# Optimization experiments

Measured on AMD Instinct MI355X. Metric: run time of the kernel, lower is better.

The kernel has to match this reference:

```python
import jax, jax.numpy as jnp
import numpy as np

D_MODEL, D_HEAD, N_HEADS, N_KV_HEADS = 4096, 128, 32, 8
EPS = 1e-5
N = 2048


def rms_norm(x, w, eps):
    return x * jax.lax.rsqrt(jnp.mean(x * x, axis=-1, keepdims=True) + eps) * w


def rope_swap(x):
    # [x0, x1, x2, x3] -> [-x1, x0, -x3, x2]
    xp = x.reshape(x.shape[:-1] + (-1, 2))
    return jnp.stack([-xp[..., 1], xp[..., 0]], axis=-1).reshape(x.shape)


def rope_rotate(x, r_cos, r_sin):
    return x * r_cos + rope_swap(x) * r_sin


def setup_inputs() -> dict:
    key = jax.random.key(0)
    ks = jax.random.split(key, 8)
    sd = 1.0 / np.sqrt(D_MODEL)
    return {
        "x": jax.random.normal(ks[0], (N, D_MODEL), dtype=jnp.float32),
        "r_cos": jax.random.normal(ks[1], (N, D_HEAD), dtype=jnp.float32),
        "r_sin": jax.random.normal(ks[2], (N, D_HEAD), dtype=jnp.float32),
        "w_norm": jnp.ones((D_MODEL,), dtype=jnp.float32),
        "wq": jax.random.normal(ks[3], (D_MODEL, N_HEADS * D_HEAD), dtype=jnp.float32) * sd,
        "wk": jax.random.normal(ks[4], (D_MODEL, N_KV_HEADS * D_HEAD), dtype=jnp.float32) * sd,
        "wv": jax.random.normal(ks[5], (D_MODEL, N_KV_HEADS * D_HEAD), dtype=jnp.float32) * sd,
        "wo": jax.random.normal(ks[6], (D_MODEL, D_MODEL), dtype=jnp.float32) * sd,
    }


def reference(x, r_cos, r_sin, w_norm, wq, wk, wv, wo):
    n = x.shape[0]
    residual = x
    h = rms_norm(x, w_norm, EPS)

    # projections -> [n_heads, n, d_head]
    q = (h @ wq).reshape(n, N_HEADS, D_HEAD).transpose(1, 0, 2)
    k = (h @ wk).reshape(n, N_KV_HEADS, D_HEAD).transpose(1, 0, 2)
    v = (h @ wv).reshape(n, N_KV_HEADS, D_HEAD).transpose(1, 0, 2)

    # GQA: repeat kv heads
    reps = N_HEADS // N_KV_HEADS
    k = jnp.repeat(k, reps, axis=0)
    v = jnp.repeat(v, reps, axis=0)

    q = rope_rotate(q, r_cos, r_sin)
    k = rope_rotate(k, r_cos, r_sin)

    mask = jnp.where(
        jnp.tril(jnp.ones((n, n), dtype=bool)), 0.0, -jnp.inf
    ).astype(x.dtype)
    scores = jnp.einsum("hnd,hmd->hnm", q, k) / np.sqrt(D_HEAD).astype(np.float32) + mask
    a = jnp.einsum("hnm,hmd->hnd", jax.nn.softmax(scores, axis=-1), v)

    a = a.transpose(1, 0, 2).reshape(n, N_HEADS * D_HEAD)
    return residual + a @ wo
```

## Files before the change

kernel.cpp:

```cpp
#include <hip/hip_runtime.h>
#include <stdint.h>
#include <math.h>

#define TOK 2048
#define DMODEL 4096
#define QKV_LD 5120
#define KVB 64
#define PS_LD 72

typedef __attribute__((ext_vector_type(8))) short short8;
typedef __attribute__((ext_vector_type(4))) short short4v;
typedef __attribute__((ext_vector_type(8))) __bf16 bf16x8;
typedef __attribute__((ext_vector_type(4))) float f32x4;

__device__ __forceinline__ unsigned short f2bf(float f) {
  unsigned u = __float_as_uint(f);
  u += 0x7fffu + ((u >> 16) & 1u);
  return (unsigned short)(u >> 16);
}

__device__ __forceinline__ void gl16(const void* g, void* l) {
  __builtin_amdgcn_global_load_lds((__attribute__((address_space(1))) void*)g,
                                   (__attribute__((address_space(3))) void*)l,
                                   16, 0, 0);
}

__device__ __forceinline__ f32x4 mfma16(short8 a, short8 b, f32x4 c) {
  return __builtin_amdgcn_mfma_f32_16x16x32_bf16(__builtin_bit_cast(bf16x8, a),
                                                 __builtin_bit_cast(bf16x8, b),
                                                 c, 0, 0, 0);
}

__device__ __forceinline__ float fexp2(float x) {
  float r;
  asm("v_exp_f32 %0, %1" : "=v"(r) : "v"(x));
  return r;
}

template <int N>
__device__ __forceinline__ void waitvm() {
  if constexpr (N == 0) asm volatile("s_waitcnt vmcnt(0)" ::: "memory");
  else if constexpr (N == 6) asm volatile("s_waitcnt vmcnt(6)" ::: "memory");
  else if constexpr (N == 7) asm volatile("s_waitcnt vmcnt(7)" ::: "memory");
  else static_assert(N == 0 || N == 6 || N == 7, "add literal");
}

__global__ __launch_bounds__(256) void k_rmsnorm(const float* __restrict__ x,
                                                 const float* __restrict__ w,
                                                 unsigned short* __restrict__ h) {
  const int row = blockIdx.x;
  const float* xr = x + (size_t)row * DMODEL;
  float4 v[4];
  float ss = 0.f;
#pragma unroll
  for (int i = 0; i < 4; ++i) {
    v[i] = *(const float4*)(xr + threadIdx.x * 4 + i * 1024);
    ss += v[i].x * v[i].x + v[i].y * v[i].y + v[i].z * v[i].z + v[i].w * v[i].w;
  }
#pragma unroll
  for (int m = 1; m < 64; m <<= 1) ss += __shfl_xor(ss, m, 64);
  __shared__ float ws4[4];
  if ((threadIdx.x & 63) == 0) ws4[threadIdx.x >> 6] = ss;
  __syncthreads();
  const float scale = rsqrtf((ws4[0] + ws4[1] + ws4[2] + ws4[3]) * (1.0f / DMODEL) + 1e-5f);
  unsigned short* hr = h + (size_t)row * DMODEL;
#pragma unroll
  for (int i = 0; i < 4; ++i) {
    int col = threadIdx.x * 4 + i * 1024;
    float4 wv = *(const float4*)(w + col);
    uint2 o;
    o.x = (unsigned)f2bf(v[i].x * scale * wv.x) | ((unsigned)f2bf(v[i].y * scale * wv.y) << 16);
    o.y = (unsigned)f2bf(v[i].z * scale * wv.z) | ((unsigned)f2bf(v[i].w * scale * wv.w) << 16);
    *(uint2*)(hr + col) = o;
  }
}

__global__ __launch_bounds__(256) void k_wconvert(const float* __restrict__ W,
                                                  unsigned short* __restrict__ WT,
                                                  int K, int N) {
  __shared__ unsigned short tile[64][65];
  const int n0 = blockIdx.x * 64, k0 = blockIdx.y * 64;
  const int t = threadIdx.x;
  {
    const int r = t >> 2, c0 = (t & 3) * 16;
    const float* src = W + (size_t)(k0 + r) * N + n0 + c0;
#pragma unroll
    for (int i = 0; i < 4; ++i) {
      float4 f = *(const float4*)(src + i * 4);
      tile[r][c0 + i * 4 + 0] = f2bf(f.x);
      tile[r][c0 + i * 4 + 1] = f2bf(f.y);
      tile[r][c0 + i * 4 + 2] = f2bf(f.z);
      tile[r][c0 + i * 4 + 3] = f2bf(f.w);
    }
  }
  __syncthreads();
  {
    const int n = t >> 2, c0 = (t & 3) * 16;
    unsigned short* dst = WT + (size_t)(n0 + n) * K + k0 + c0;
    unsigned short v[16];
#pragma unroll
    for (int i = 0; i < 16; ++i) v[i] = tile[c0 + i][n];
    uint4 o0, o1;
    o0.x = v[0] | ((unsigned)v[1] << 16);  o0.y = v[2] | ((unsigned)v[3] << 16);
    o0.z = v[4] | ((unsigned)v[5] << 16);  o0.w = v[6] | ((unsigned)v[7] << 16);
    o1.x = v[8] | ((unsigned)v[9] << 16);  o1.y = v[10] | ((unsigned)v[11] << 16);
    o1.z = v[12] | ((unsigned)v[13] << 16); o1.w = v[14] | ((unsigned)v[15] << 16);
    *(uint4*)dst = o0;
    *(uint4*)(dst + 8) = o1;
  }
}

__device__ __forceinline__ short8 rdfrag(const unsigned short* buf, int row, int kc) {
  return *(const short8*)((const char*)buf + row * 128 + ((kc ^ (row & 7)) << 4));
}

template <int BM, int BN>
__device__ __forceinline__ void stage_tile(const unsigned short* __restrict__ A,
                                           const unsigned short* __restrict__ BT,
                                           unsigned short* __restrict__ buf,
                                           int m0, int n0, int K, int kt, int tid) {
  constexpr int ALOADS = BM * 8 / 512;
  constexpr int BLOADS = BN * 8 / 512;
  unsigned short* bbuf = buf + BM * 64;
#pragma unroll
  for (int i = 0; i < ALOADS; ++i) {
    const int s = i * 512 + tid, row = s >> 3, ch = s & 7;
    gl16(A + (size_t)(m0 + row) * K + kt + ((ch ^ (row & 7)) << 3), (char*)buf + s * 16);
  }
#pragma unroll
  for (int i = 0; i < BLOADS; ++i) {
    const int s = i * 512 + tid, row = s >> 3, ch = s & 7;
    gl16(BT + (size_t)(n0 + row) * K + kt + ((ch ^ (row & 7)) << 3), (char*)bbuf + s * 16);
  }
}

template <int BM, int BN, int MODE, int GXLOG>
__global__ __launch_bounds__(512, 2) void k_gemm_big(const unsigned short* __restrict__ A,
                                                     const unsigned short* __restrict__ BT,
                                                     const float* __restrict__ resid,
                                                     void* __restrict__ Cout,
                                                     unsigned short* __restrict__ vtg,
                                                     int M, int N, int K) {
  extern __shared__ __align__(16) unsigned short lds[];
  constexpr int MREP = BM / 32;
  constexpr int NREP = BN / 64;
  constexpr int TILE = (BM + BN) * 64;
  constexpr int LOADS = (BM + BN) / 64;

  const int tid = threadIdx.x, lane = tid & 63;
  const int w = tid >> 6, wm = w >> 2, wn = w & 3;
  const int lr = lane & 15, lh = lane >> 4;

  const int nwg = gridDim.x * gridDim.y;
  const int wg0 = blockIdx.y * gridDim.x + blockIdx.x;
  const int swz = (wg0 & 7) * (nwg >> 3) + (wg0 >> 3);
  const int m0 = (swz >> GXLOG) * BM;
  const int n0 = (swz & ((1 << GXLOG) - 1)) * BN;

  const f32x4 zf = {0.f, 0.f, 0.f, 0.f};
  f32x4 acc[MREP][NREP];
#pragma unroll
  for (int i = 0; i < MREP; ++i) {
#pragma unroll
    for (int j = 0; j < NREP; ++j) acc[i][j] = zf;
  }

  const int arow0 = wm * (BM / 2);
  const int brow0 = wn * (BN / 4);
  const int NT = K >> 6;
  int cur = 0;

  stage_tile<BM, BN>(A, BT, lds, m0, n0, K, 0, tid);

  for (int t = 0; t < NT; ++t) {
    const unsigned short* abuf = lds + cur * TILE;
    const unsigned short* bbuf = abuf + BM * 64;
    if (t + 1 < NT) {
      stage_tile<BM, BN>(A, BT, lds + (cur ^ 1) * TILE, m0, n0, K, (t + 1) << 6, tid);
      waitvm<LOADS>();
    } else {
      waitvm<0>();
    }
    __builtin_amdgcn_s_barrier();
    __builtin_amdgcn_sched_barrier(0);

    short8 bfr[NREP][2];
#pragma unroll
    for (int nr = 0; nr < NREP; ++nr) {
#pragma unroll
      for (int kk = 0; kk < 2; ++kk)
        bfr[nr][kk] = rdfrag(bbuf, brow0 + nr * 16 + lr, kk * 4 + lh);
    }
#pragma unroll
    for (int mp = 0; mp < 4; ++mp) {
      short8 afr[2][2];
#pragma unroll
      for (int mi = 0; mi < 2; ++mi) {
#pragma unroll
        for (int kk = 0; kk < 2; ++kk)
          afr[mi][kk] = rdfrag(abuf, arow0 + (mp * 2 + mi) * 16 + lr, kk * 4 + lh);
      }
      __builtin_amdgcn_s_setprio(1);
#pragma unroll
      for (int mi = 0; mi < 2; ++mi) {
#pragma unroll
        for (int nr = 0; nr < NREP; ++nr) {
#pragma unroll
          for (int kk = 0; kk < 2; ++kk)
            acc[mp * 2 + mi][nr] = mfma16(afr[mi][kk], bfr[nr][kk], acc[mp * 2 + mi][nr]);
        }
      }
      __builtin_amdgcn_s_setprio(0);
    }
    __builtin_amdgcn_sched_barrier(0);
    __builtin_amdgcn_s_barrier();
    cur ^= 1;
  }

#pragma unroll
  for (int ai = 0; ai < MREP; ++ai) {
#pragma unroll
    for (int ni = 0; ni < NREP; ++ni) {
      const int colg = n0 + wn * (BN / 4) + ni * 16 + lr;
      const int rowg0 = m0 + wm * (BM / 2) + ai * 16 + 4 * lh;
      if (MODE == 1) {
#pragma unroll
        for (int r = 0; r < 4; ++r)
          ((float*)Cout)[(size_t)(rowg0 + r) * N + colg] =
              acc[ai][ni][r] + resid[(size_t)(rowg0 + r) * N + colg];
      } else if (colg >= 5120) {
        short4v o;
#pragma unroll
        for (int r = 0; r < 4; ++r) o[r] = (short)f2bf(acc[ai][ni][r]);
        *(short4v*)(vtg + (size_t)(colg - 5120) * TOK + rowg0) = o;
      } else {
#pragma unroll
        for (int r = 0; r < 4; ++r)
          ((unsigned short*)Cout)[(size_t)(rowg0 + r) * QKV_LD + colg] = f2bf(acc[ai][ni][r]);
      }
    }
  }
}

__global__ __launch_bounds__(256) void k_rope(unsigned short* __restrict__ qkv,
                                              const float* __restrict__ rc,
                                              const float* __restrict__ rs) {
  const int row = blockIdx.y;
  const int p = blockIdx.x * 256 + threadIdx.x;
  const int col = p * 2;
  const int d = col & 127;
  unsigned short* ptr = qkv + (size_t)row * QKV_LD + col;
  const unsigned both = *(const unsigned*)ptr;
  const float x0 = __uint_as_float((both & 0xffffu) << 16);
  const float x1 = __uint_as_float(both & 0xffff0000u);
  const float c0 = rc[row * 128 + d], c1 = rc[row * 128 + d + 1];
  const float s0 = rs[row * 128 + d], s1 = rs[row * 128 + d + 1];
  const float y0 = x0 * c0 - x1 * s0;
  const float y1 = x1 * c1 + x0 * s1;
  *(unsigned*)ptr = (unsigned)f2bf(y0) | ((unsigned)f2bf(y1) << 16);
}

__global__ __launch_bounds__(256) void k_attn(const unsigned short* __restrict__ qkv,
                                              const unsigned short* __restrict__ vtg,
                                              unsigned short* __restrict__ aout) {
  __shared__ __align__(16) unsigned short Ks[KVB * 128];
  __shared__ __align__(16) unsigned short Vt[128 * KVB];
  __shared__ __align__(16) unsigned short Ps[4][16 * PS_LD];
  const int head = blockIdx.y;
  const int hkv = head >> 2;
  const int tid = threadIdx.x, lane = tid & 63, w = tid >> 6;
  const int lr = lane & 15, lh = lane >> 4;
  const float scale2 = 0.08838834764831845f * 1.44269504088896340736f;
  const f32x4 zf = {0.f, 0.f, 0.f, 0.f};

  for (int half = 0; half < 2; ++half) {
    const int qt = half ? (31 - blockIdx.x) : blockIdx.x;
    const int q0 = qt * 64;

    short8 qf[4];
    {
      const unsigned short* qbase = qkv + (size_t)(q0 + w * 16 + lr) * QKV_LD + head * 128;
#pragma unroll
      for (int kd = 0; kd < 4; ++kd) qf[kd] = *(const short8*)(qbase + kd * 32 + lh * 8);
    }
    f32x4 oacc[8];
#pragma unroll
    for (int vt = 0; vt < 8; ++vt) oacc[vt] = zf;
    float Mr[4], Lr[4];
#pragma unroll
    for (int r = 0; r < 4; ++r) { Mr[r] = -INFINITY; Lr[r] = 0.f; }

    const int nt = qt + 1;
    for (int t = 0; t < nt; ++t) {
      const int kv0 = t * KVB;
      __syncthreads();
#pragma unroll
      for (int c = 0; c < 4; ++c) {
        const int s = c * 256 + w * 64 + lane;
        const int row = s >> 4, cp = s & 15;
        gl16(qkv + (size_t)(kv0 + row) * QKV_LD + 4096 + hkv * 128 + ((cp ^ (row & 7)) * 8),
             (char*)Ks + (c * 256 + w * 64) * 16);
      }
#pragma unroll
      for (int c = 0; c < 4; ++c) {
        const int s = c * 256 + w * 64 + lane;
        const int row = s >> 3, cp = s & 7;
        gl16(vtg + (size_t)(hkv * 128 + row) * TOK + kv0 + ((cp ^ (row & 7)) * 8),
             (char*)Vt + (c * 256 + w * 64) * 16);
      }
      __syncthreads();

      f32x4 sacc[4];
#pragma unroll
      for (int ct = 0; ct < 4; ++ct) {
        sacc[ct] = zf;
        const int row = ct * 16 + lr;
#pragma unroll
        for (int kd = 0; kd < 4; ++kd) {
          const short8 kf = *(const short8*)((const char*)Ks + row * 256 +
                                             (((kd * 4 + lh) ^ (row & 7)) * 16));
          sacc[ct] = mfma16(qf[kd], kf, sacc[ct]);
        }
      }

      float scv[4], pv[4][4];
#pragma unroll
      for (int r = 0; r < 4; ++r) {
        const int qrow = q0 + w * 16 + 4 * lh + r;
        float s0 = sacc[0][r] * scale2;
        float s1 = sacc[1][r] * scale2;
        float s2 = sacc[2][r] * scale2;
        float s3 = sacc[3][r] * scale2;
        if (kv0 + lr > qrow) s0 = -INFINITY;
        if (kv0 + 16 + lr > qrow) s1 = -INFINITY;
        if (kv0 + 32 + lr > qrow) s2 = -INFINITY;
        if (kv0 + 48 + lr > qrow) s3 = -INFINITY;
        float tmax = fmaxf(fmaxf(s0, s1), fmaxf(s2, s3));
        tmax = fmaxf(tmax, __shfl_xor(tmax, 1, 16));
        tmax = fmaxf(tmax, __shfl_xor(tmax, 2, 16));
        tmax = fmaxf(tmax, __shfl_xor(tmax, 4, 16));
        tmax = fmaxf(tmax, __shfl_xor(tmax, 8, 16));
        const float mnew = fmaxf(Mr[r], tmax);
        const float sc = fexp2(Mr[r] - mnew);
        Mr[r] = mnew;
        const float p0 = fexp2(s0 - mnew);
        const float p1 = fexp2(s1 - mnew);
        const float p2 = fexp2(s2 - mnew);
        const float p3 = fexp2(s3 - mnew);
        float ps = (p0 + p1) + (p2 + p3);
        ps += __shfl_xor(ps, 1, 16);
        ps += __shfl_xor(ps, 2, 16);
        ps += __shfl_xor(ps, 4, 16);
        ps += __shfl_xor(ps, 8, 16);
        Lr[r] = Lr[r] * sc + ps;
        scv[r] = sc;
        pv[r][0] = p0; pv[r][1] = p1; pv[r][2] = p2; pv[r][3] = p3;
      }
#pragma unroll
      for (int vt = 0; vt < 8; ++vt) {
#pragma unroll
        for (int r = 0; r < 4; ++r) oacc[vt][r] *= scv[r];
      }

      unsigned short* pw = Ps[w];
#pragma unroll
      for (int r = 0; r < 4; ++r) {
#pragma unroll
        for (int ct = 0; ct < 4; ++ct)
          pw[(4 * lh + r) * PS_LD + ct * 16 + lr] = f2bf(pv[r][ct]);
      }
      asm volatile("s_waitcnt lgkmcnt(0)" ::: "memory");
      short8 pf[2];
      pf[0] = *(const short8*)(pw + lr * PS_LD + lh * 8);
      pf[1] = *(const short8*)(pw + lr * PS_LD + 32 + lh * 8);
      __builtin_amdgcn_s_setprio(1);
#pragma unroll
      for (int vt = 0; vt < 8; ++vt) {
        const int d = vt * 16 + lr;
#pragma unroll
        for (int kb = 0; kb < 2; ++kb) {
          const short8 vf = *(const short8*)((const char*)Vt + d * 128 +
                                             (((kb * 4 + lh) ^ (lr & 7)) * 16));
          oacc[vt] = mfma16(pf[kb], vf, oacc[vt]);
        }
      }
      __builtin_amdgcn_s_setprio(0);
    }

#pragma unroll
    for (int r = 0; r < 4; ++r) {
      const float inv = 1.0f / Lr[r];
      const size_t rowoff = (size_t)(q0 + w * 16 + 4 * lh + r) * DMODEL + head * 128;
#pragma unroll
      for (int vt = 0; vt < 8; ++vt)
        aout[rowoff + vt * 16 + lr] = f2bf(oacc[vt][r] * inv);
    }
  }
}

extern "C" void kernel_launch(void* const* d_in, const int* in_sizes, int n_in,
                              void* d_out, int out_size, void* d_ws, size_t ws_size,
                              hipStream_t stream) {
  (void)in_sizes; (void)n_in; (void)out_size; (void)ws_size;
  const float* x     = (const float*)d_in[0];
  const float* r_cos = (const float*)d_in[1];
  const float* r_sin = (const float*)d_in[2];
  const float* wnorm = (const float*)d_in[3];
  const float* wq    = (const float*)d_in[4];
  const float* wk    = (const float*)d_in[5];
  const float* wv    = (const float*)d_in[6];
  const float* wo    = (const float*)d_in[7];

  unsigned short* bufA = (unsigned short*)d_ws;
  unsigned short* qkvb = bufA + (size_t)TOK * DMODEL;
  unsigned short* wT   = qkvb + (size_t)TOK * QKV_LD;
  unsigned short* vtg  = wT + (size_t)6144 * DMODEL;

  hipFuncSetAttribute((const void*)k_gemm_big<256, 192, 0, 5>,
                      hipFuncAttributeMaxDynamicSharedMemorySize, 4 * (256 + 192) * 64);
  hipFuncSetAttribute((const void*)k_gemm_big<256, 128, 1, 5>,
                      hipFuncAttributeMaxDynamicSharedMemorySize, 4 * (256 + 128) * 64);

  k_rmsnorm<<<TOK, 256, 0, stream>>>(x, wnorm, bufA);
  k_wconvert<<<dim3(64, 64), 256, 0, stream>>>(wq, wT, DMODEL, 4096);
  k_wconvert<<<dim3(16, 64), 256, 0, stream>>>(wk, wT + (size_t)4096 * DMODEL, DMODEL, 1024);
  k_wconvert<<<dim3(16, 64), 256, 0, stream>>>(wv, wT + (size_t)5120 * DMODEL, DMODEL, 1024);
  k_gemm_big<256, 192, 0, 5><<<dim3(256), 512, 4 * (256 + 192) * 64, stream>>>(
      bufA, wT, nullptr, qkvb, vtg, TOK, 6144, DMODEL);
  k_wconvert<<<dim3(64, 64), 256, 0, stream>>>(wo, wT, DMODEL, 4096);
  k_rope<<<dim3(10, TOK), 256, 0, stream>>>(qkvb, r_cos, r_sin);
  k_attn<<<dim3(16, 32), 256, 0, stream>>>(qkvb, vtg, bufA);
  k_gemm_big<256, 128, 1, 5><<<dim3(256), 512, 4 * (256 + 128) * 64, stream>>>(
      bufA, wT, x, d_out, nullptr, TOK, DMODEL, DMODEL);
}
```

Measured before the change: 342.0 us.

## Interleave next-tile global loads with MFMA phases and remap blocks per XCD

The GEMM main loop no longer issues the whole next-tile prefetch up front and then waits on a vmcnt. It now splits the prefetch into two halves, issued during the first two of four MFMA sub-phases, with barriers between phases and a full __syncthreads at the end of each K step. The block-to-tile mapping is also changed so that each XCD gets a contiguous 4x8 patch of output tiles, meant to improve L2 reuse. The per-phase barriers add synchronisation cost, and because the end-of-step __syncthreads replaces the explicit vmcnt wait, the loop now relies on the compiler emitting vmcnt(0) before that barrier for the LDS data to be correct.

Result: faster. 334.7 us (-2.1%).

```diff
diff --git a/kernel.cpp b/kernel.cpp
--- a/kernel.cpp
+++ b/kernel.cpp
@@ -35,14 +35,6 @@
   float r;
   asm("v_exp_f32 %0, %1" : "=v"(r) : "v"(x));
   return r;
-}
-
-template <int N>
-__device__ __forceinline__ void waitvm() {
-  if constexpr (N == 0) asm volatile("s_waitcnt vmcnt(0)" ::: "memory");
-  else if constexpr (N == 6) asm volatile("s_waitcnt vmcnt(6)" ::: "memory");
-  else if constexpr (N == 7) asm volatile("s_waitcnt vmcnt(7)" ::: "memory");
-  else static_assert(N == 0 || N == 6 || N == 7, "add literal");
 }
 
 __global__ __launch_bounds__(256) void k_rmsnorm(const float* __restrict__ x,
@@ -114,27 +106,28 @@
   return *(const short8*)((const char*)buf + row * 128 + ((kc ^ (row & 7)) << 4));
 }
 
-template <int BM, int BN>
-__device__ __forceinline__ void stage_tile(const unsigned short* __restrict__ A,
+template <int BM, int BN, int HALF>
+__device__ __forceinline__ void stage_half(const unsigned short* __restrict__ A,
                                            const unsigned short* __restrict__ BT,
                                            unsigned short* __restrict__ buf,
                                            int m0, int n0, int K, int kt, int tid) {
-  constexpr int ALOADS = BM * 8 / 512;
-  constexpr int BLOADS = BN * 8 / 512;
+  constexpr int AL = BM / 64, BL = BN / 64;
+  constexpr int A0 = HALF ? AL / 2 : 0, A1 = HALF ? AL : AL / 2;
+  constexpr int B0 = HALF ? BL / 2 : 0, B1 = HALF ? BL : BL / 2;
   unsigned short* bbuf = buf + BM * 64;
 #pragma unroll
-  for (int i = 0; i < ALOADS; ++i) {
+  for (int i = A0; i < A1; ++i) {
     const int s = i * 512 + tid, row = s >> 3, ch = s & 7;
     gl16(A + (size_t)(m0 + row) * K + kt + ((ch ^ (row & 7)) << 3), (char*)buf + s * 16);
   }
 #pragma unroll
-  for (int i = 0; i < BLOADS; ++i) {
+  for (int i = B0; i < B1; ++i) {
     const int s = i * 512 + tid, row = s >> 3, ch = s & 7;
     gl16(BT + (size_t)(n0 + row) * K + kt + ((ch ^ (row & 7)) << 3), (char*)bbuf + s * 16);
   }
 }
 
-template <int BM, int BN, int MODE, int GXLOG>
+template <int BM, int BN, int MODE>
 __global__ __launch_bounds__(512, 2) void k_gemm_big(const unsigned short* __restrict__ A,
                                                      const unsigned short* __restrict__ BT,
                                                      const float* __restrict__ resid,
@@ -145,17 +138,15 @@
   constexpr int MREP = BM / 32;
   constexpr int NREP = BN / 64;
   constexpr int TILE = (BM + BN) * 64;
-  constexpr int LOADS = (BM + BN) / 64;
 
   const int tid = threadIdx.x, lane = tid & 63;
   const int w = tid >> 6, wm = w >> 2, wn = w & 3;
   const int lr = lane & 15, lh = lane >> 4;
 
-  const int nwg = gridDim.x * gridDim.y;
-  const int wg0 = blockIdx.y * gridDim.x + blockIdx.x;
-  const int swz = (wg0 & 7) * (nwg >> 3) + (wg0 >> 3);
-  const int m0 = (swz >> GXLOG) * BM;
-  const int n0 = (swz & ((1 << GXLOG) - 1)) * BN;
+  const int wg0 = blockIdx.x;
+  const int xcd = wg0 & 7, l = wg0 >> 3;
+  const int m0 = (((xcd >> 2) << 2) + (l >> 3)) * BM;
+  const int n0 = (((xcd & 3) << 3) + (l & 7)) * BN;
 
   const f32x4 zf = {0.f, 0.f, 0.f, 0.f};
   f32x4 acc[MREP][NREP];
@@ -170,19 +161,16 @@
   const int NT = K >> 6;
   int cur = 0;
 
-  stage_tile<BM, BN>(A, BT, lds, m0, n0, K, 0, tid);
+  stage_half<BM, BN, 0>(A, BT, lds, m0, n0, K, 0, tid);
+  stage_half<BM, BN, 1>(A, BT, lds, m0, n0, K, 0, tid);
+  __syncthreads();
 
   for (int t = 0; t < NT; ++t) {
     const unsigned short* abuf = lds + cur * TILE;
     const unsigned short* bbuf = abuf + BM * 64;
-    if (t + 1 < NT) {
-      stage_tile<BM, BN>(A, BT, lds + (cur ^ 1) * TILE, m0, n0, K, (t + 1) << 6, tid);
-      waitvm<LOADS>();
-    } else {
-      waitvm<0>();
-    }
-    __builtin_amdgcn_s_barrier();
-    __builtin_amdgcn_sched_barrier(0);
+    unsigned short* nbuf = lds + (cur ^ 1) * TILE;
+    const bool pre = (t + 1 < NT);
+    const int ktn = (t + 1) << 6;
 
     short8 bfr[NREP][2];
 #pragma unroll
@@ -191,15 +179,19 @@
       for (int kk = 0; kk < 2; ++kk)
         bfr[nr][kk] = rdfrag(bbuf, brow0 + nr * 16 + lr, kk * 4 + lh);
     }
-#pragma unroll
-    for (int mp = 0; mp < 4; ++mp) {
+
+#pragma unroll
+    for (int p = 0; p < 4; ++p) {
       short8 afr[2][2];
 #pragma unroll
       for (int mi = 0; mi < 2; ++mi) {
 #pragma unroll
         for (int kk = 0; kk < 2; ++kk)
-          afr[mi][kk] = rdfrag(abuf, arow0 + (mp * 2 + mi) * 16 + lr, kk * 4 + lh);
-      }
+          afr[mi][kk] = rdfrag(abuf, arow0 + (p * 2 + mi) * 16 + lr, kk * 4 + lh);
+      }
+      if (p == 0 && pre) stage_half<BM, BN, 0>(A, BT, nbuf, m0, n0, K, ktn, tid);
+      if (p == 1 && pre) stage_half<BM, BN, 1>(A, BT, nbuf, m0, n0, K, ktn, tid);
+      __builtin_amdgcn_s_barrier();
       __builtin_amdgcn_s_setprio(1);
 #pragma unroll
       for (int mi = 0; mi < 2; ++mi) {
@@ -207,13 +199,13 @@
         for (int nr = 0; nr < NREP; ++nr) {
 #pragma unroll
           for (int kk = 0; kk < 2; ++kk)
-            acc[mp * 2 + mi][nr] = mfma16(afr[mi][kk], bfr[nr][kk], acc[mp * 2 + mi][nr]);
+            acc[p * 2 + mi][nr] = mfma16(afr[mi][kk], bfr[nr][kk], acc[p * 2 + mi][nr]);
         }
       }
       __builtin_amdgcn_s_setprio(0);
-    }
-    __builtin_amdgcn_sched_barrier(0);
-    __builtin_amdgcn_s_barrier();
+      if (p < 3) __builtin_amdgcn_s_barrier();
+    }
+    __syncthreads();
     cur ^= 1;
   }
 
@@ -416,20 +408,20 @@
   unsigned short* wT   = qkvb + (size_t)TOK * QKV_LD;
   unsigned short* vtg  = wT + (size_t)6144 * DMODEL;
 
-  hipFuncSetAttribute((const void*)k_gemm_big<256, 192, 0, 5>,
+  hipFuncSetAttribute((const void*)k_gemm_big<256, 192, 0>,
                       hipFuncAttributeMaxDynamicSharedMemorySize, 4 * (256 + 192) * 64);
-  hipFuncSetAttribute((const void*)k_gemm_big<256, 128, 1, 5>,
+  hipFuncSetAttribute((const void*)k_gemm_big<256, 128, 1>,
                       hipFuncAttributeMaxDynamicSharedMemorySize, 4 * (256 + 128) * 64);
 
   k_rmsnorm<<<TOK, 256, 0, stream>>>(x, wnorm, bufA);
   k_wconvert<<<dim3(64, 64), 256, 0, stream>>>(wq, wT, DMODEL, 4096);
   k_wconvert<<<dim3(16, 64), 256, 0, stream>>>(wk, wT + (size_t)4096 * DMODEL, DMODEL, 1024);
   k_wconvert<<<dim3(16, 64), 256, 0, stream>>>(wv, wT + (size_t)5120 * DMODEL, DMODEL, 1024);
-  k_gemm_big<256, 192, 0, 5><<<dim3(256), 512, 4 * (256 + 192) * 64, stream>>>(
+  k_gemm_big<256, 192, 0><<<dim3(256), 512, 4 * (256 + 192) * 64, stream>>>(
       bufA, wT, nullptr, qkvb, vtg, TOK, 6144, DMODEL);
   k_wconvert<<<dim3(64, 64), 256, 0, stream>>>(wo, wT, DMODEL, 4096);
   k_rope<<<dim3(10, TOK), 256, 0, stream>>>(qkvb, r_cos, r_sin);
   k_attn<<<dim3(16, 32), 256, 0, stream>>>(qkvb, vtg, bufA);
-  k_gemm_big<256, 128, 1, 5><<<dim3(256), 512, 4 * (256 + 128) * 64, stream>>>(
+  k_gemm_big<256, 128, 1><<<dim3(256), 512, 4 * (256 + 128) * 64, stream>>>(
       bufA, wT, x, d_out, nullptr, TOK, DMODEL, DMODEL);
 }
```
